# Kernel optimization log

Measured on AMD Instinct MI355X. Metric: run time of the kernel, lower is better.

Reference implementation:

```python
import jax, jax.numpy as jnp
import numpy as np

E, QE, P, H = 3, 60000, 40, 20   # elements, atoms per element, fp length, hidden
NIMG = 1800                       # images in batch
Q = E * QE                        # total atoms
NNZ = 14_400_000                  # nnz of sparse fprimes [P*Q, 3*Q]


def setup_inputs() -> dict:
    key = jax.random.key(0)
    ks = jax.random.split(key, 12)
    fps = jax.random.normal(ks[0], (E, QE, P), jnp.float32)
    image_idx = jax.random.randint(ks[1], (E, QE), 0, NIMG, jnp.int32)
    s1 = 1.0 / np.sqrt(P)
    s2 = 1.0 / np.sqrt(H)
    W1 = (jax.random.normal(ks[2], (E, P, H)) * s1).astype(jnp.float32)
    b1 = jnp.zeros((E, H), jnp.float32)
    W2 = (jax.random.normal(ks[3], (E, H, H)) * s2).astype(jnp.float32)
    b2 = jnp.zeros((E, H), jnp.float32)
    W3 = (jax.random.normal(ks[4], (E, H, 1)) * s2).astype(jnp.float32)
    b3 = jnp.zeros((E, 1), jnp.float32)
    fp_rows = jax.random.randint(ks[5], (NNZ,), 0, P * Q, jnp.int32)
    fp_cols = jax.random.randint(ks[6], (NNZ,), 0, 3 * Q, jnp.int32)
    fp_vals = (jax.random.normal(ks[7], (NNZ,)) * 0.05).astype(jnp.float32)
    return {"fps": fps, "W1": W1, "b1": b1, "W2": W2, "b2": b2, "W3": W3,
            "b3": b3, "image_idx": image_idx, "fp_rows": fp_rows,
            "fp_cols": fp_cols, "fp_vals": fp_vals, "batch_size": NIMG}


def _mlp(x, w1, b1, w2, b2, w3, b3):
    # Dense(tanh) -> Dense(tanh) -> Dense(linear), per amptorch MLP(n_layers=3)
    h = jnp.tanh(x @ w1 + b1)
    h = jnp.tanh(h @ w2 + b2)
    return h @ w3 + b3  # [..., 1]


def _esum(x, w1, b1, w2, b2, w3, b3):
    return _mlp(x, w1, b1, w2, b2, w3, b3).sum()


def reference(fps, W1, b1, W2, b2, W3, b3, image_idx, fp_rows, fp_cols,
              fp_vals, batch_size):
    # per-element atomwise energies: [E, QE, 1]
    atom_e = jax.vmap(_mlp)(fps, W1, b1, W2, b2, W3, b3)
    # scatter-add atomic energies into per-image energies (index_add_)
    energy_pred = jax.ops.segment_sum(
        atom_e.reshape(-1, 1), image_idx.reshape(-1).astype(jnp.int32),
        num_segments=batch_size)  # [NIMG, 1]
    # dE/dFP per atom (each atom's output depends only on its own fp, so
    # grad of the per-element energy sum == per-atom jacobian rows)
    dE_dFP = jax.vmap(jax.grad(_esum))(fps, W1, b1, W2, b2, W3, b3)  # [E,QE,P]
    # reorder atoms from element-grouped order to image-index order
    # (stable argsort == boolean-match reorder in the torch code)
    order = jnp.argsort(image_idx.reshape(-1))
    dE_flat = dE_dFP.reshape(-1, P)[order].reshape(-1)  # [P*Q]
    # force = -fprimes^T @ dE_dFP  (sparse COO matvec via segment_sum)
    force_flat = -jax.ops.segment_sum(
        fp_vals * dE_flat[fp_rows], fp_cols, num_segments=3 * Q)
    force_pred = force_flat.reshape(-1, 3)  # [Q, 3]
    return energy_pred, force_pred
```

## Files before the change

kernel.cpp:

```cpp
#include <hip/hip_runtime.h>
#include <math.h>

#define E_    3
#define QE_   60000
#define QTOT  180000
#define P_    40
#define H_    20
#define NIMG_ 1800
#define NNZ_  14400000
#define BLK   256
#define NB    704

#define CW_BITS 12
#define CW      4096
#define NBIN    132
#define SUBS    8
#define SC      8192
#define NSB     1758

typedef int   vi4 __attribute__((ext_vector_type(4)));
typedef float vf4 __attribute__((ext_vector_type(4)));

__global__ void zero_kernel(float* __restrict__ out, int n) {
    int i = blockIdx.x * blockDim.x + threadIdx.x;
    if (i < n) out[i] = 0.0f;
}

__global__ void hist_kernel(const int* __restrict__ img, int* __restrict__ g_hist) {
    __shared__ int h[NIMG_];
    const int t = threadIdx.x, b = blockIdx.x;
    for (int v = t; v < NIMG_; v += BLK) h[v] = 0;
    __syncthreads();
    int a = b * BLK + t;
    if (a < QTOT) atomicAdd(&h[img[a]], 1);
    __syncthreads();
    for (int v = t; v < NIMG_; v += BLK) g_hist[v * NB + b] = h[v];
}

__global__ void scan_blocks_kernel(int* __restrict__ g_hist, int* __restrict__ g_total) {
    __shared__ int s[BLK];
    const int v = blockIdx.x, t = threadIdx.x;
    int carry = 0;
    for (int c = 0; c < NB; c += BLK) {
        int idx = c + t;
        int val = (idx < NB) ? g_hist[v * NB + idx] : 0;
        s[t] = val; __syncthreads();
        for (int off = 1; off < BLK; off <<= 1) {
            int tmp = (t >= off) ? s[t - off] : 0;
            __syncthreads();
            s[t] += tmp;
            __syncthreads();
        }
        int excl = s[t] - val;
        int tot  = s[BLK - 1];
        if (idx < NB) g_hist[v * NB + idx] = carry + excl;
        carry += tot;
        __syncthreads();
    }
// ... 83 lines not shown
    float ea = sB3;
    #pragma unroll
    for (int i = 0; i < H_; ++i) ea += h2v[i] * sW3[i];
    atomicAdd(&energy[img[a]], ea);

    float dz2[H_];
    #pragma unroll
    for (int i = 0; i < H_; ++i) dz2[i] = sW3[i] * (1.0f - h2v[i] * h2v[i]);
    float dz1[H_];
    #pragma unroll
    for (int i = 0; i < H_; ++i) {
        float d = 0.0f;
        #pragma unroll
        for (int j = 0; j < H_; ++j) d += sW2[i * H_ + j] * dz2[j];
        dz1[i] = d * (1.0f - h1v[i] * h1v[i]);
    }
    float* op = dEflat + (size_t)rank[a] * P_;
    #pragma unroll
    for (int p = 0; p < P_; p += 4) {
        float4 v4;
        float d0 = 0.f, d1 = 0.f, d2 = 0.f, d3 = 0.f;
        #pragma unroll
        for (int i = 0; i < H_; ++i) {
            d0 += sW1[(p    ) * H_ + i] * dz1[i];
            d1 += sW1[(p + 1) * H_ + i] * dz1[i];
            d2 += sW1[(p + 2) * H_ + i] * dz1[i];
            d3 += sW1[(p + 3) * H_ + i] * dz1[i];
        }
        v4.x = d0; v4.y = d1; v4.z = d2; v4.w = d3;
        *(float4*)(op + p) = v4;
    }
}

__global__ __launch_bounds__(BLK) void fhist_kernel(const int* __restrict__ cols,
                                                    int* __restrict__ binHist) {
    __shared__ int h[NBIN];
    const int t = threadIdx.x, b = blockIdx.x;
    if (t < NBIN) h[t] = 0;
    __syncthreads();
    const int base = b * SC;
    if (base + SC <= NNZ_) {
        const vi4* c4 = (const vi4*)(cols + base);
        #pragma unroll
        for (int j = 0; j < SC / (BLK * 4); ++j) {
            vi4 cc = __builtin_nontemporal_load(c4 + j * BLK + t);
            atomicAdd(&h[cc.x >> CW_BITS], 1);
            atomicAdd(&h[cc.y >> CW_BITS], 1);
            atomicAdd(&h[cc.z >> CW_BITS], 1);
            atomicAdd(&h[cc.w >> CW_BITS], 1);
        }
    } else {
        for (int j = 0; j < SC / BLK; ++j) {
            int k = base + j * BLK + t;
            if (k < NNZ_) atomicAdd(&h[cols[k] >> CW_BITS], 1);
        }
    }
    __syncthreads();
    if (t < NBIN) binHist[t * NSB + b] = h[t];
}

__global__ void fscan_blocks_kernel(int* __restrict__ binHist, int* __restrict__ binTotal) {
    __shared__ int s[BLK];
    const int v = blockIdx.x, t = threadIdx.x;
    int carry = 0;
    for (int c = 0; c < NSB; c += BLK) {
        int idx = c + t;
        int val = (idx < NSB) ? binHist[v * NSB + idx] : 0;
        s[t] = val; __syncthreads();
        for (int off = 1; off < BLK; off <<= 1) {
            int tmp = (t >= off) ? s[t - off] : 0;
            __syncthreads();
            s[t] += tmp;
            __syncthreads();
        }
        int excl = s[t] - val;
        int tot  = s[BLK - 1];
        if (idx < NSB) binHist[v * NSB + idx] = carry + excl;
        carry += tot;
        __syncthreads();
    }
    if (t == 0) binTotal[v] = carry;
}

__global__ void fbase_kernel(const int* __restrict__ binTotal, int* __restrict__ binBase) {
    __shared__ int s[BLK];
    const int t = threadIdx.x;
    int v = (t < NBIN) ? binTotal[t] : 0;
    s[t] = v; __syncthreads();
    for (int off = 1; off < BLK; off <<= 1) {
        int tmp = (t >= off) ? s[t - off] : 0;
        __syncthreads();
        s[t] += tmp;
        __syncthreads();
    }
    if (t < NBIN) binBase[t] = s[t] - v;
    if (t == 0) binBase[NBIN] = s[BLK - 1];
}

__global__ __launch_bounds__(BLK) void fscatter_kernel(
    const int* __restrict__ rows, const int* __restrict__ cols, const float* __restrict__ vals,
    const float* __restrict__ dEflat, const int* __restrict__ binHist,
    const int* __restrict__ binBase, unsigned* __restrict__ bm)
{
    __shared__ unsigned items[SC];
    __shared__ unsigned char bins[SC];
    __shared__ int hist[NBIN];
    __shared__ int cursor[NBIN];
    __shared__ int delta[NBIN];
    __shared__ int s[BLK];
    const int t = threadIdx.x, b = blockIdx.x;
    const int base = b * SC;
    const int nIt = min(SC, NNZ_ - base);
    const bool full = (base + SC <= NNZ_);

    if (t < NBIN) hist[t] = 0;
    __syncthreads();

    if (full) {
        const vi4* c4 = (const vi4*)(cols + base);
        #pragma unroll
        for (int j = 0; j < SC / (BLK * 4); ++j) {
            vi4 cc = __builtin_nontemporal_load(c4 + j * BLK + t);
            atomicAdd(&hist[cc.x >> CW_BITS], 1);
            atomicAdd(&hist[cc.y >> CW_BITS], 1);
            atomicAdd(&hist[cc.z >> CW_BITS], 1);
            atomicAdd(&hist[cc.w >> CW_BITS], 1);
        }
    } else {
        for (int j = 0; j < SC / BLK; ++j) {
            int k = base + j * BLK + t;
            if (k < NNZ_) atomicAdd(&hist[cols[k] >> CW_BITS], 1);
        }
    }
    __syncthreads();

    {
        int v = (t < NBIN) ? hist[t] : 0;
        s[t] = v; __syncthreads();
        for (int off = 1; off < BLK; off <<= 1) {
            int tmp = (t >= off) ? s[t - off] : 0;
            __syncthreads();
            s[t] += tmp;
            __syncthreads();
        }
        if (t < NBIN) {
            int ls = s[t] - v;
            cursor[t] = ls;
            delta[t]  = binBase[t] + binHist[t * NSB + b] - ls;
        }
    }
    __syncthreads();

    if (full) {
        const vi4* c4 = (const vi4*)(cols + base);
        const vi4* r4 = (const vi4*)(rows + base);
        const vf4* v4 = (const vf4*)(vals + base);
        #pragma unroll 2
        for (int j = 0; j < SC / (BLK * 4); ++j) {
            int idx = j * BLK + t;
            vi4 cc = __builtin_nontemporal_load(c4 + idx);
            vi4 rr = __builtin_nontemporal_load(r4 + idx);
            vf4 vv = __builtin_nontemporal_load(v4 + idx);
            float d0 = dEflat[rr.x];
            float d1 = dEflat[rr.y];
            float d2 = dEflat[rr.z];
            float d3 = dEflat[rr.w];
            #define PLACE(CI, VI, DI)                                              \
            {                                                                      \
                int bin = (CI) >> CW_BITS;                                         \
                unsigned u = __float_as_uint(-(VI) * (DI));                        \
                unsigned pk = ((unsigned)((CI) & (CW - 1)) << 20)                  \
                            | ((u + 0x800u) >> 12);                                \
                int pos = atomicAdd(&cursor[bin], 1);                              \
                items[pos] = pk;                                                   \
                bins[pos] = (unsigned char)bin;                                    \
            }
            PLACE(cc.x, vv.x, d0)
            PLACE(cc.y, vv.y, d1)
            PLACE(cc.z, vv.z, d2)
            PLACE(cc.w, vv.w, d3)
        }
    } else {
        for (int j = 0; j < SC / BLK; ++j) {
            int k = base + j * BLK + t;
            if (k < NNZ_) {
                int c = cols[k];
                float d = dEflat[rows[k]];
                float v = vals[k];
                PLACE(c, v, d)
            }
        }
    }
    __syncthreads();

    for (int i = t; i < nIt; i += BLK) {
        __builtin_nontemporal_store(items[i], &bm[delta[bins[i]] + i]);
    }
}

__global__ __launch_bounds__(BLK) void fforce_kernel(
    const unsigned* __restrict__ bm, const int* __restrict__ binBase,
    float* __restrict__ partial)
{
    __shared__ float w[CW];
    const int t = threadIdx.x;
    const int bin = blockIdx.x >> 3;
    const int sub = blockIdx.x & (SUBS - 1);
    for (int i = t; i < CW; i += BLK) w[i] = 0.0f;
    __syncthreads();
    const int start = binBase[bin];
    const int cnt   = binBase[bin + 1] - start;
    const int sBeg  = start + (cnt * sub) / SUBS;
    const int sEnd  = start + (cnt * (sub + 1)) / SUBS;
    int i = sBeg + t;
    for (; i + 3 * BLK < sEnd; i += 4 * BLK) {
        unsigned p0 = __builtin_nontemporal_load(bm + i);
        unsigned p1 = __builtin_nontemporal_load(bm + i + BLK);
        unsigned p2 = __builtin_nontemporal_load(bm + i + 2 * BLK);
        unsigned p3 = __builtin_nontemporal_load(bm + i + 3 * BLK);
        atomicAdd(&w[p0 >> 20], __uint_as_float((p0 & 0xFFFFFu) << 12));
        atomicAdd(&w[p1 >> 20], __uint_as_float((p1 & 0xFFFFFu) << 12));
        atomicAdd(&w[p2 >> 20], __uint_as_float((p2 & 0xFFFFFu) << 12));
        atomicAdd(&w[p3 >> 20], __uint_as_float((p3 & 0xFFFFFu) << 12));
    }
    for (; i < sEnd; i += BLK) {
        unsigned p = bm[i];
        atomicAdd(&w[p >> 20], __uint_as_float((p & 0xFFFFFu) << 12));
    }
    __syncthreads();
    float* dst = partial + (size_t)blockIdx.x * CW;
    for (int k = t; k < CW; k += BLK) __builtin_nontemporal_store(w[k], dst + k);
}

__global__ void freduce_kernel(const float* __restrict__ partial, float* __restrict__ force) {
    int i = blockIdx.x * BLK + threadIdx.x;
    if (i < 3 * QTOT) {
        int bin = i >> CW_BITS, local = i & (CW - 1);
        const float* p = partial + (size_t)bin * (CW * SUBS) + local;
        float sum = 0.0f;
        #pragma unroll
        for (int k = 0; k < SUBS; ++k) sum += __builtin_nontemporal_load(p + k * CW);
        force[i] = sum;
    }
}

__global__ void force_kernel(const int* __restrict__ rows, const int* __restrict__ cols,
                             const float* __restrict__ vals, const float* __restrict__ dEflat,
                             float* __restrict__ force) {
    int k = blockIdx.x * blockDim.x + threadIdx.x;
    if (k < NNZ_) {
        float contrib = -vals[k] * dEflat[rows[k]];
        atomicAdd(&force[cols[k]], contrib);
    }
}

extern "C" void kernel_launch(void* const* d_in, const int* in_sizes, int n_in,
                              void* d_out, int out_size, void* d_ws, size_t ws_size,
                              hipStream_t stream) {
    (void)in_sizes; (void)n_in; (void)out_size;
    const float* fps  = (const float*)d_in[0];
    const float* W1   = (const float*)d_in[1];
    const float* b1   = (const float*)d_in[2];
    const float* W2   = (const float*)d_in[3];
    const float* b2   = (const float*)d_in[4];
    const float* W3   = (const float*)d_in[5];
    const float* b3   = (const float*)d_in[6];
    const int*   img  = (const int*)d_in[7];
    const int*   rows = (const int*)d_in[8];
    const int*   cols = (const int*)d_in[9];
    const float* vals = (const float*)d_in[10];

    char* ws = (char*)d_ws;
    int*   g_hist  = (int*)(ws);
    int*   g_total = (int*)(ws + 5068800);
    int*   g_base  = (int*)(ws + 5076000);
    int*   rank    = (int*)(ws + 5083200);
    float* dEflat  = (float*)(ws + 5803200);
    int*      binHist  = (int*)(ws + 34603200);
    int*      binTotal = (int*)(ws + 35531424);
    int*      binBase  = (int*)(ws + 35531952);
    unsigned* bm       = (unsigned*)(ws + 35532496);
    float*    partial  = (float*)(ws + 93132496);
    const size_t WS_NEEDED = 110434000;

    float* energy = (float*)d_out;
    float* force  = (float*)d_out + NIMG_;

    const int nOut = NIMG_ + 3 * QTOT;
    zero_kernel<<<(nOut + BLK - 1) / BLK, BLK, 0, stream>>>((float*)d_out, nOut);

    hist_kernel<<<NB, BLK, 0, stream>>>(img, g_hist);
    scan_blocks_kernel<<<NIMG_, BLK, 0, stream>>>(g_hist, g_total);
    scan_buckets_kernel<<<1, BLK, 0, stream>>>(g_total, g_base);
    rank_kernel<<<NB, BLK, 0, stream>>>(img, g_hist, g_base, rank);

    dim3 gm((QE_ + BLK - 1) / BLK, E_);
    mlp_kernel<<<gm, BLK, 0, stream>>>(fps, W1, b1, W2, b2, W3, b3, img, rank,
                                       energy, dEflat);

    if (ws_size >= WS_NEEDED) {
        fhist_kernel<<<NSB, BLK, 0, stream>>>(cols, binHist);
        fscan_blocks_kernel<<<NBIN, BLK, 0, stream>>>(binHist, binTotal);
        fbase_kernel<<<1, BLK, 0, stream>>>(binTotal, binBase);
        fscatter_kernel<<<NSB, BLK, 0, stream>>>(rows, cols, vals, dEflat,
                                                 binHist, binBase, bm);
        fforce_kernel<<<NBIN * SUBS, BLK, 0, stream>>>(bm, binBase, partial);
        freduce_kernel<<<(3 * QTOT + BLK - 1) / BLK, BLK, 0, stream>>>(partial, force);
    } else {
        force_kernel<<<NNZ_ / BLK, BLK, 0, stream>>>(rows, cols, vals, dEflat, force);
    }
}
```

Before: 647.7 us.

## Pre-sort nnz by row slice so dEflat gathers stay L2-local

Adds a new force path that first buckets nonzeros into 55 row slices (slice histogram, plan, per-block slice sort). Each entry is stored as a packed (15-bit value, local row) word plus its column. The column-binned scatter then runs per slice, with each group of blocks working on one slice, so the random dEflat gathers hit a small window that fits in cache. The cost is an extra full pass that reads and writes all 14.4M nnz, several more kernel launches, a larger workspace, and value precision cut to about 15 bits.

```diff
diff --git a/kernel.cpp b/kernel.cpp
--- a/kernel.cpp
+++ b/kernel.cpp
@@ -18,12 +18,33 @@
 #define SC      8192
 #define NSB     1758
 
+#define SLICE_SHIFT 17
+#define NSLICE  55
+#define MAXCH   1813
+#define FS_GRID 768
+#define FS_PERX 96
+
+#define C_CNT   0
+#define C_SBASE 64
+#define C_SCUR  128
+#define C_TOT   184
+#define C_CHS   192
+#define C_CHST  2048
+#define C_CHLEN 4096
+#define C_GRP   6144
+#define C_GCNT  8192
+#define C_INTS  8448
+
 typedef int   vi4 __attribute__((ext_vector_type(4)));
 typedef float vf4 __attribute__((ext_vector_type(4)));
+typedef unsigned uint32;
 
 __global__ void zero_kernel(float* __restrict__ out, int n) {
     int i = blockIdx.x * blockDim.x + threadIdx.x;
     if (i < n) out[i] = 0.0f;
+}
+__global__ void zero_ctrl_kernel(int* __restrict__ ctrl) {
+    ctrl[threadIdx.x] = 0;
 }
 
 __global__ void hist_kernel(const int* __restrict__ img, int* __restrict__ g_hist) {
@@ -173,40 +194,208 @@
     }
 }
 
-__global__ __launch_bounds__(BLK) void fhist_kernel(const int* __restrict__ cols,
-                                                    int* __restrict__ binHist) {
-    __shared__ int h[NBIN];
+
+__global__ __launch_bounds__(BLK) void slice_hist_kernel(const int* __restrict__ rows,
+                                                         int* __restrict__ ctrl) {
+    __shared__ int h[NSLICE];
     const int t = threadIdx.x, b = blockIdx.x;
-    if (t < NBIN) h[t] = 0;
+    if (t < NSLICE) h[t] = 0;
     __syncthreads();
     const int base = b * SC;
     if (base + SC <= NNZ_) {
-        const vi4* c4 = (const vi4*)(cols + base);
+        const vi4* r4 = (const vi4*)(rows + base);
         #pragma unroll
         for (int j = 0; j < SC / (BLK * 4); ++j) {
-            vi4 cc = __builtin_nontemporal_load(c4 + j * BLK + t);
-            atomicAdd(&h[cc.x >> CW_BITS], 1);
-            atomicAdd(&h[cc.y >> CW_BITS], 1);
-            atomicAdd(&h[cc.z >> CW_BITS], 1);
-            atomicAdd(&h[cc.w >> CW_BITS], 1);
+            vi4 rr = __builtin_nontemporal_load(r4 + j * BLK + t);
+            atomicAdd(&h[rr.x >> SLICE_SHIFT], 1);
+            atomicAdd(&h[rr.y >> SLICE_SHIFT], 1);
+            atomicAdd(&h[rr.z >> SLICE_SHIFT], 1);
+            atomicAdd(&h[rr.w >> SLICE_SHIFT], 1);
         }
     } else {
         for (int j = 0; j < SC / BLK; ++j) {
             int k = base + j * BLK + t;
-            if (k < NNZ_) atomicAdd(&h[cols[k] >> CW_BITS], 1);
-        }
-    }
-    __syncthreads();
-    if (t < NBIN) binHist[t * NSB + b] = h[t];
-}
-
-__global__ void fscan_blocks_kernel(int* __restrict__ binHist, int* __restrict__ binTotal) {
+            if (k < NNZ_) atomicAdd(&h[rows[k] >> SLICE_SHIFT], 1);
+        }
+    }
+    __syncthreads();
+    if (t < NSLICE && h[t] > 0) atomicAdd(&ctrl[C_CNT + t], h[t]);
+}
+
+__global__ void plan_kernel(int* __restrict__ ctrl) {
+    __shared__ int scnt[NSLICE], sb[NSLICE + 1], cb[NSLICE + 1], gp[NSLICE];
+    __shared__ int g8[8], tot_s;
+    const int t = threadIdx.x;
+    if (t < NSLICE) scnt[t] = ctrl[C_CNT + t];
+    __syncthreads();
+    if (t == 0) {
+        int run = 0, crun = 0;
+        int gs[8]; for (int x = 0; x < 8; ++x) gs[x] = 0;
+        for (int s = 0; s < NSLICE; ++s) {
+            sb[s] = run;
+            run += scnt[s];
+            run = (run + 3) & ~3;
+            int nc = (scnt[s] + SC - 1) / SC;
+            cb[s] = crun; crun += nc;
+            int x = s & 7;
+            gp[s] = gs[x]; gs[x] += nc;
+        }
+        sb[NSLICE] = run; cb[NSLICE] = crun; tot_s = crun;
+        for (int x = 0; x < 8; ++x) g8[x] = gs[x];
+    }
+    __syncthreads();
+    const int tot = tot_s;
+    if (t < NSLICE) { ctrl[C_SBASE + t] = sb[t]; ctrl[C_SCUR + t] = sb[t]; }
+    if (t == 0) { ctrl[C_SBASE + NSLICE] = sb[NSLICE]; ctrl[C_TOT] = tot; }
+    if (t < 8) ctrl[C_GCNT + t] = g8[t];
+    for (int idx = t; idx < MAXCH; idx += BLK) {
+        if (idx < tot) {
+            int s = 0;
+            for (int k = 0; k < NSLICE; ++k) if (cb[k] <= idx) s = k;
+            int c = idx - cb[s];
+            ctrl[C_CHS + idx]   = s;
+            ctrl[C_CHST + idx]  = sb[s] + c * SC;
+            ctrl[C_CHLEN + idx] = min(SC, scnt[s] - c * SC);
+            ctrl[C_GRP + (s & 7) * 256 + gp[s] + c] = idx;
+        } else {
+            ctrl[C_CHS + idx] = 0; ctrl[C_CHST + idx] = 0; ctrl[C_CHLEN + idx] = 0;
+        }
+    }
+}
+
+__global__ __launch_bounds__(BLK) void slice_sort_kernel(
+    const int* __restrict__ rows, const int* __restrict__ cols, const float* __restrict__ vals,
+    int* __restrict__ ctrl, uint32* __restrict__ itemX, uint32* __restrict__ itemY)
+{
+    __shared__ uint32 rbuf[SC];
+    __shared__ uint32 sbuf[SC];
+    __shared__ int h[NSLICE], lb[NSLICE + 1], res[NSLICE], cur[NSLICE];
+    const int t = threadIdx.x, b = blockIdx.x;
+    const int base = b * SC;
+    const int len = min(SC, NNZ_ - base);
+    const bool full = (len == SC);
+
+    if (t < NSLICE) h[t] = 0;
+    __syncthreads();
+    if (full) {
+        const vi4* r4 = (const vi4*)(rows + base);
+        #pragma unroll
+        for (int j = 0; j < SC / (BLK * 4); ++j) {
+            int idx = j * BLK + t;
+            vi4 rr = __builtin_nontemporal_load(r4 + idx);
+            rbuf[idx * 4 + 0] = (uint32)rr.x; atomicAdd(&h[rr.x >> SLICE_SHIFT], 1);
+            rbuf[idx * 4 + 1] = (uint32)rr.y; atomicAdd(&h[rr.y >> SLICE_SHIFT], 1);
+            rbuf[idx * 4 + 2] = (uint32)rr.z; atomicAdd(&h[rr.z >> SLICE_SHIFT], 1);
+            rbuf[idx * 4 + 3] = (uint32)rr.w; atomicAdd(&h[rr.w >> SLICE_SHIFT], 1);
+        }
+    } else {
+        for (int j = t; j < len; j += BLK) {
+            int r = rows[base + j];
+            rbuf[j] = (uint32)r;
+            atomicAdd(&h[r >> SLICE_SHIFT], 1);
+        }
+    }
+    __syncthreads();
+    if (t == 0) {
+        int run = 0;
+        for (int s = 0; s < NSLICE; ++s) { lb[s] = run; run += h[s]; }
+        lb[NSLICE] = run;
+    }
+    __syncthreads();
+    if (t < NSLICE) {
+        cur[t] = lb[t];
+        res[t] = (h[t] > 0) ? atomicAdd(&ctrl[C_SCUR + t], h[t]) : 0;
+    }
+    __syncthreads();
+    for (int j = t; j < len; j += BLK) {
+        uint32 r = rbuf[j];
+        int bn = (int)(r >> SLICE_SHIFT);
+        int pos = atomicAdd(&cur[bn], 1);
+        sbuf[pos] = ((uint32)j << SLICE_SHIFT) | (r & 0x1FFFFu);
+    }
+    __syncthreads();
+    if (full) {
+        const vi4* v4 = (const vi4*)(vals + base);
+        #pragma unroll
+        for (int j = 0; j < SC / (BLK * 4); ++j) {
+            int idx = j * BLK + t;
+            vi4 vv = __builtin_nontemporal_load(v4 + idx);
+            rbuf[idx * 4 + 0] = (uint32)vv.x; rbuf[idx * 4 + 1] = (uint32)vv.y;
+            rbuf[idx * 4 + 2] = (uint32)vv.z; rbuf[idx * 4 + 3] = (uint32)vv.w;
+        }
+    } else {
+        for (int j = t; j < len; j += BLK) rbuf[j] = ((const uint32*)vals)[base + j];
+    }
+    __syncthreads();
+    for (int j = t; j < len; j += BLK) {
+        uint32 e = sbuf[j];
+        int i = (int)(e >> SLICE_SHIFT);
+        uint32 rl = e & 0x1FFFFu;
+        uint32 v15 = (rbuf[i] + 0x10000u) >> 17;
+        int lo = 0, hi = NSLICE;
+        while (hi - lo > 1) { int mid = (lo + hi) >> 1; if (lb[mid] <= j) lo = mid; else hi = mid; }
+        int dst = res[lo] + (j - lb[lo]);
+        itemX[dst] = (v15 << 17) | rl;
+    }
+    __syncthreads();
+    if (full) {
+        const vi4* c4 = (const vi4*)(cols + base);
+        #pragma unroll
+        for (int j = 0; j < SC / (BLK * 4); ++j) {
+            int idx = j * BLK + t;
+            vi4 cc = __builtin_nontemporal_load(c4 + idx);
+            rbuf[idx * 4 + 0] = (uint32)cc.x; rbuf[idx * 4 + 1] = (uint32)cc.y;
+            rbuf[idx * 4 + 2] = (uint32)cc.z; rbuf[idx * 4 + 3] = (uint32)cc.w;
+        }
+    } else {
+        for (int j = t; j < len; j += BLK) rbuf[j] = (uint32)cols[base + j];
+    }
+    __syncthreads();
+    for (int j = t; j < len; j += BLK) {
+        uint32 e = sbuf[j];
+        int i = (int)(e >> SLICE_SHIFT);
+        int lo = 0, hi = NSLICE;
+        while (hi - lo > 1) { int mid = (lo + hi) >> 1; if (lb[mid] <= j) lo = mid; else hi = mid; }
+        int dst = res[lo] + (j - lb[lo]);
+        itemY[dst] = rbuf[i];
+    }
+}
+
+__global__ __launch_bounds__(BLK) void fhist3_kernel(const uint32* __restrict__ itemY,
+                                                     const int* __restrict__ ctrl,
+                                                     int* __restrict__ binHist) {
+    __shared__ int h[NBIN];
+    const int t = threadIdx.x, g = blockIdx.x;
+    if (t < NBIN) h[t] = 0;
+    __syncthreads();
+    const int start = ctrl[C_CHST + g];
+    const int len   = ctrl[C_CHLEN + g];
+    if (len == SC) {
+        const vi4* y4 = (const vi4*)(itemY + start);
+        #pragma unroll
+        for (int j = 0; j < SC / (BLK * 4); ++j) {
+            vi4 yy = __builtin_nontemporal_load(y4 + j * BLK + t);
+            atomicAdd(&h[yy.x >> CW_BITS], 1);
+            atomicAdd(&h[yy.y >> CW_BITS], 1);
+            atomicAdd(&h[yy.z >> CW_BITS], 1);
+            atomicAdd(&h[yy.w >> CW_BITS], 1);
+        }
+    } else {
+        for (int j = t; j < len; j += BLK)
+            atomicAdd(&h[itemY[start + j] >> CW_BITS], 1);
+    }
+    __syncthreads();
+    if (t < NBIN) binHist[t * MAXCH + g] = h[t];
+}
+
+__global__ void fscan_blocks_kernel(int* __restrict__ binHist, int* __restrict__ binTotal,
+                                    int n) {
     __shared__ int s[BLK];
     const int v = blockIdx.x, t = threadIdx.x;
     int carry = 0;
-    for (int c = 0; c < NSB; c += BLK) {
+    for (int c = 0; c < n; c += BLK) {
         int idx = c + t;
-        int val = (idx < NSB) ? binHist[v * NSB + idx] : 0;
+        int val = (idx < n) ? binHist[v * n + idx] : 0;
         s[t] = val; __syncthreads();
         for (int off = 1; off < BLK; off <<= 1) {
             int tmp = (t >= off) ? s[t - off] : 0;
@@ -216,7 +405,7 @@
         }
         int excl = s[t] - val;
         int tot  = s[BLK - 1];
-        if (idx < NSB) binHist[v * NSB + idx] = carry + excl;
+        if (idx < n) binHist[v * n + idx] = carry + excl;
         carry += tot;
         __syncthreads();
     }
@@ -238,12 +427,184 @@
     if (t == 0) binBase[NBIN] = s[BLK - 1];
 }
 
+__global__ __launch_bounds__(BLK) void fscatter3_kernel(
+    const uint32* __restrict__ itemX, const uint32* __restrict__ itemY,
+    const float* __restrict__ dEflat, const int* __restrict__ ctrl,
+    const int* __restrict__ binHist, const int* __restrict__ binBase,
+    uint32* __restrict__ bm)
+{
+    __shared__ uint32 items[SC];
+    __shared__ unsigned char bns[SC];
+    __shared__ int h[NBIN], cur[NBIN], dlt[NBIN];
+    __shared__ int sc[BLK];
+    const int t = threadIdx.x;
+    const int x = blockIdx.x & 7;
+    const int r = blockIdx.x >> 3;
+    const int gc = ctrl[C_GCNT + x];
+
+    for (int w = r; w < gc; w += FS_PERX) {
+        const int g     = ctrl[C_GRP + x * 256 + w];
+        const int sl    = ctrl[C_CHS + g];
+        const int start = ctrl[C_CHST + g];
+        const int len   = ctrl[C_CHLEN + g];
+        const int row0  = sl << SLICE_SHIFT;
+
+        if (t < NBIN) h[t] = 0;
+        __syncthreads();
+        if (len == SC) {
+            const vi4* y4 = (const vi4*)(itemY + start);
+            #pragma unroll
+            for (int j = 0; j < SC / (BLK * 4); ++j) {
+                vi4 yy = __builtin_nontemporal_load(y4 + j * BLK + t);
+                atomicAdd(&h[yy.x >> CW_BITS], 1);
+                atomicAdd(&h[yy.y >> CW_BITS], 1);
+                atomicAdd(&h[yy.z >> CW_BITS], 1);
+                atomicAdd(&h[yy.w >> CW_BITS], 1);
+            }
+        } else {
+            for (int j = t; j < len; j += BLK)
+                atomicAdd(&h[itemY[start + j] >> CW_BITS], 1);
+        }
+        __syncthreads();
+        {
+            int v = (t < NBIN) ? h[t] : 0;
+            sc[t] = v; __syncthreads();
+            for (int off = 1; off < BLK; off <<= 1) {
+                int tmp = (t >= off) ? sc[t - off] : 0;
+                __syncthreads();
+                sc[t] += tmp;
+                __syncthreads();
+            }
+            if (t < NBIN) {
+                int ls = sc[t] - v;
+                cur[t] = ls;
+                dlt[t] = binBase[t] + binHist[t * MAXCH + g] - ls;
+            }
+        }
+        __syncthreads();
+        if (len == SC) {
+            const vi4* x4 = (const vi4*)(itemX + start);
+            const vi4* y4 = (const vi4*)(itemY + start);
+            #pragma unroll 2
+            for (int j = 0; j < SC / (BLK * 4); ++j) {
+                int idx = j * BLK + t;
+                vi4 xx = __builtin_nontemporal_load(x4 + idx);
+                vi4 yy = __builtin_nontemporal_load(y4 + idx);
+                float d0 = dEflat[row0 + (((uint32)xx.x) & 0x1FFFFu)];
+                float d1 = dEflat[row0 + (((uint32)xx.y) & 0x1FFFFu)];
+                float d2 = dEflat[row0 + (((uint32)xx.z) & 0x1FFFFu)];
+                float d3 = dEflat[row0 + (((uint32)xx.w) & 0x1FFFFu)];
+                #define PLACE3(XI, YI, DI)                                         \
+                {                                                                  \
+                    uint32 col = (uint32)(YI);                                     \
+                    int bin = (int)(col >> CW_BITS);                               \
+                    float val = __uint_as_float((((uint32)(XI)) >> 17) << 17);     \
+                    uint32 u = __float_as_uint(-val * (DI));                       \
+                    uint32 pk = ((col & (CW - 1)) << 20) | ((u + 0x800u) >> 12);   \
+                    int pos = atomicAdd(&cur[bin], 1);                             \
+                    items[pos] = pk;                                               \
+                    bns[pos] = (unsigned char)bin;                                 \
+                }
+                PLACE3(xx.x, yy.x, d0)
+                PLACE3(xx.y, yy.y, d1)
+                PLACE3(xx.z, yy.z, d2)
+                PLACE3(xx.w, yy.w, d3)
+            }
+        } else {
+            for (int j = t; j < len; j += BLK) {
+                uint32 xi = itemX[start + j];
+                uint32 yi = itemY[start + j];
+                float d = dEflat[row0 + (xi & 0x1FFFFu)];
+                PLACE3(xi, yi, d)
+            }
+        }
+        __syncthreads();
+        for (int i = t; i < len; i += BLK) {
+            __builtin_nontemporal_store(items[i], &bm[dlt[bns[i]] + i]);
+        }
+        __syncthreads();
+    }
+}
+
+__global__ __launch_bounds__(BLK) void fforce_kernel(
+    const uint32* __restrict__ bm, const int* __restrict__ binBase,
+    float* __restrict__ partial)
+{
+    __shared__ float w[CW];
+    const int t = threadIdx.x;
+    const int bin = blockIdx.x >> 3;
+    const int sub = blockIdx.x & (SUBS - 1);
+    for (int i = t; i < CW; i += BLK) w[i] = 0.0f;
+    __syncthreads();
+    const int start = binBase[bin];
+    const int cnt   = binBase[bin + 1] - start;
+    const int sBeg  = start + (cnt * sub) / SUBS;
+    const int sEnd  = start + (cnt * (sub + 1)) / SUBS;
+    int i = sBeg + t;
+    for (; i + 3 * BLK < sEnd; i += 4 * BLK) {
+        uint32 p0 = __builtin_nontemporal_load(bm + i);
+        uint32 p1 = __builtin_nontemporal_load(bm + i + BLK);
+        uint32 p2 = __builtin_nontemporal_load(bm + i + 2 * BLK);
+        uint32 p3 = __builtin_nontemporal_load(bm + i + 3 * BLK);
+        atomicAdd(&w[p0 >> 20], __uint_as_float((p0 & 0xFFFFFu) << 12));
+        atomicAdd(&w[p1 >> 20], __uint_as_float((p1 & 0xFFFFFu) << 12));
+        atomicAdd(&w[p2 >> 20], __uint_as_float((p2 & 0xFFFFFu) << 12));
+        atomicAdd(&w[p3 >> 20], __uint_as_float((p3 & 0xFFFFFu) << 12));
+    }
+    for (; i < sEnd; i += BLK) {
+        uint32 p = bm[i];
+        atomicAdd(&w[p >> 20], __uint_as_float((p & 0xFFFFFu) << 12));
+    }
+    __syncthreads();
+    float* dst = partial + (size_t)blockIdx.x * CW;
+    for (int k = t; k < CW; k += BLK) __builtin_nontemporal_store(w[k], dst + k);
+}
+
+__global__ void freduce_kernel(const float* __restrict__ partial, float* __restrict__ force) {
+    int i = blockIdx.x * BLK + threadIdx.x;
+    if (i < 3 * QTOT) {
+        int bin = i >> CW_BITS, local = i & (CW - 1);
+        const float* p = partial + (size_t)bin * (CW * SUBS) + local;
+        float sum = 0.0f;
+        #pragma unroll
+        for (int k = 0; k < SUBS; ++k) sum += __builtin_nontemporal_load(p + k * CW);
+        force[i] = sum;
+    }
+}
+
+__global__ __launch_bounds__(BLK) void fhist_kernel(const int* __restrict__ cols,
+                                                    int* __restrict__ binHist) {
+    __shared__ int h[NBIN];
+    const int t = threadIdx.x, b = blockIdx.x;
+    if (t < NBIN) h[t] = 0;
+    __syncthreads();
+    const int base = b * SC;
+    if (base + SC <= NNZ_) {
+        const vi4* c4 = (const vi4*)(cols + base);
+        #pragma unroll
+        for (int j = 0; j < SC / (BLK * 4); ++j) {
+            vi4 cc = __builtin_nontemporal_load(c4 + j * BLK + t);
+            atomicAdd(&h[cc.x >> CW_BITS], 1);
+            atomicAdd(&h[cc.y >> CW_BITS], 1);
+            atomicAdd(&h[cc.z >> CW_BITS], 1);
+            atomicAdd(&h[cc.w >> CW_BITS], 1);
+        }
+    } else {
+        for (int j = 0; j < SC / BLK; ++j) {
+            int k = base + j * BLK + t;
+            if (k < NNZ_) atomicAdd(&h[cols[k] >> CW_BITS], 1);
+        }
+    }
+    __syncthreads();
+    if (t < NBIN) binHist[t * NSB + b] = h[t];
+}
+
 __global__ __launch_bounds__(BLK) void fscatter_kernel(
     const int* __restrict__ rows, const int* __restrict__ cols, const float* __restrict__ vals,
     const float* __restrict__ dEflat, const int* __restrict__ binHist,
-    const int* __restrict__ binBase, unsigned* __restrict__ bm)
+    const int* __restrict__ binBase, uint32* __restrict__ bm)
 {
-    __shared__ unsigned items[SC];
+    __shared__ uint32 items[SC];
     __shared__ unsigned char bins[SC];
     __shared__ int hist[NBIN];
     __shared__ int cursor[NBIN];
@@ -256,7 +617,6 @@
 
     if (t < NBIN) hist[t] = 0;
     __syncthreads();
-
     if (full) {
         const vi4* c4 = (const vi4*)(cols + base);
         #pragma unroll
@@ -274,7 +634,6 @@
         }
     }
     __syncthreads();
-
     {
         int v = (t < NBIN) ? hist[t] : 0;
         s[t] = v; __syncthreads();
@@ -291,7 +650,6 @@
         }
     }
     __syncthreads();
-
     if (full) {
         const vi4* c4 = (const vi4*)(cols + base);
         const vi4* r4 = (const vi4*)(rows + base);
@@ -309,8 +667,8 @@
             #define PLACE(CI, VI, DI)                                              \
             {                                                                      \
                 int bin = (CI) >> CW_BITS;                                         \
-                unsigned u = __float_as_uint(-(VI) * (DI));                        \
-                unsigned pk = ((unsigned)((CI) & (CW - 1)) << 20)                  \
+                uint32 u = __float_as_uint(-(VI) * (DI));                          \
+                uint32 pk = ((uint32)((CI) & (CW - 1)) << 20)                      \
                             | ((u + 0x800u) >> 12);                                \
                 int pos = atomicAdd(&cursor[bin], 1);                              \
                 items[pos] = pk;                                                   \
@@ -333,55 +691,8 @@
         }
     }
     __syncthreads();
-
     for (int i = t; i < nIt; i += BLK) {
         __builtin_nontemporal_store(items[i], &bm[delta[bins[i]] + i]);
-    }
-}
-
-__global__ __launch_bounds__(BLK) void fforce_kernel(
-    const unsigned* __restrict__ bm, const int* __restrict__ binBase,
-    float* __restrict__ partial)
-{
-    __shared__ float w[CW];
-    const int t = threadIdx.x;
-    const int bin = blockIdx.x >> 3;
-    const int sub = blockIdx.x & (SUBS - 1);
-    for (int i = t; i < CW; i += BLK) w[i] = 0.0f;
-    __syncthreads();
-    const int start = binBase[bin];
-    const int cnt   = binBase[bin + 1] - start;
-    const int sBeg  = start + (cnt * sub) / SUBS;
-    const int sEnd  = start + (cnt * (sub + 1)) / SUBS;
-    int i = sBeg + t;
-    for (; i + 3 * BLK < sEnd; i += 4 * BLK) {
-        unsigned p0 = __builtin_nontemporal_load(bm + i);
-        unsigned p1 = __builtin_nontemporal_load(bm + i + BLK);
-        unsigned p2 = __builtin_nontemporal_load(bm + i + 2 * BLK);
-        unsigned p3 = __builtin_nontemporal_load(bm + i + 3 * BLK);
-        atomicAdd(&w[p0 >> 20], __uint_as_float((p0 & 0xFFFFFu) << 12));
-        atomicAdd(&w[p1 >> 20], __uint_as_float((p1 & 0xFFFFFu) << 12));
-        atomicAdd(&w[p2 >> 20], __uint_as_float((p2 & 0xFFFFFu) << 12));
-        atomicAdd(&w[p3 >> 20], __uint_as_float((p3 & 0xFFFFFu) << 12));
-    }
-    for (; i < sEnd; i += BLK) {
-        unsigned p = bm[i];
-        atomicAdd(&w[p >> 20], __uint_as_float((p & 0xFFFFFu) << 12));
-    }
-    __syncthreads();
-    float* dst = partial + (size_t)blockIdx.x * CW;
-    for (int k = t; k < CW; k += BLK) __builtin_nontemporal_store(w[k], dst + k);
-}
-
-__global__ void freduce_kernel(const float* __restrict__ partial, float* __restrict__ force) {
-    int i = blockIdx.x * BLK + threadIdx.x;
-    if (i < 3 * QTOT) {
-        int bin = i >> CW_BITS, local = i & (CW - 1);
-        const float* p = partial + (size_t)bin * (CW * SUBS) + local;
-        float sum = 0.0f;
-        #pragma unroll
-        for (int k = 0; k < SUBS; ++k) sum += __builtin_nontemporal_load(p + k * CW);
-        force[i] = sum;
     }
 }
 
@@ -417,12 +728,6 @@
     int*   g_base  = (int*)(ws + 5076000);
     int*   rank    = (int*)(ws + 5083200);
     float* dEflat  = (float*)(ws + 5803200);
-    int*      binHist  = (int*)(ws + 34603200);
-    int*      binTotal = (int*)(ws + 35531424);
-    int*      binBase  = (int*)(ws + 35531952);
-    unsigned* bm       = (unsigned*)(ws + 35532496);
-    float*    partial  = (float*)(ws + 93132496);
-    const size_t WS_NEEDED = 110434000;
 
     float* energy = (float*)d_out;
     float* force  = (float*)d_out + NIMG_;
@@ -439,14 +744,43 @@
     mlp_kernel<<<gm, BLK, 0, stream>>>(fps, W1, b1, W2, b2, W3, b3, img, rank,
                                        energy, dEflat);
 
-    if (ws_size >= WS_NEEDED) {
-        fhist_kernel<<<NSB, BLK, 0, stream>>>(cols, binHist);
-        fscan_blocks_kernel<<<NBIN, BLK, 0, stream>>>(binHist, binTotal);
-        fbase_kernel<<<1, BLK, 0, stream>>>(binTotal, binBase);
+    int*    binHist3  = (int*)(ws + 34603200);
+    int*    binTotal3 = (int*)(ws + 35560464);
+    int*    binBase3  = (int*)(ws + 35560992);
+    int*    ctrl      = (int*)(ws + 35563136);
+    uint32* itemX     = (uint32*)(ws + 35596928);
+    uint32* itemY     = (uint32*)(ws + 93198976);
+    uint32* bm3       = (uint32*)(ws + 150801024);
+    float*  partial3  = (float*)(ws + 35596928);
+    const size_t WS_V3 = 208401024;
+
+    int*    binHist5  = (int*)(ws + 34603200);
+    int*    binTotal5 = (int*)(ws + 35531424);
+    int*    binBase5  = (int*)(ws + 35531952);
+    uint32* bm5       = (uint32*)(ws + 35532496);
+    float*  partial5  = (float*)(ws + 93132496);
+    const size_t WS_V2 = 110434000;
+
+    if (ws_size >= WS_V3) {
+        zero_ctrl_kernel<<<1, 256, 0, stream>>>(ctrl);
+        slice_hist_kernel<<<NSB, BLK, 0, stream>>>(rows, ctrl);
+        plan_kernel<<<1, BLK, 0, stream>>>(ctrl);
+        slice_sort_kernel<<<NSB, BLK, 0, stream>>>(rows, cols, vals, ctrl, itemX, itemY);
+        fhist3_kernel<<<MAXCH, BLK, 0, stream>>>(itemY, ctrl, binHist3);
+        fscan_blocks_kernel<<<NBIN, BLK, 0, stream>>>(binHist3, binTotal3, MAXCH);
+        fbase_kernel<<<1, BLK, 0, stream>>>(binTotal3, binBase3);
+        fscatter3_kernel<<<FS_GRID, BLK, 0, stream>>>(itemX, itemY, dEflat, ctrl,
+                                                      binHist3, binBase3, bm3);
+        fforce_kernel<<<NBIN * SUBS, BLK, 0, stream>>>(bm3, binBase3, partial3);
+        freduce_kernel<<<(3 * QTOT + BLK - 1) / BLK, BLK, 0, stream>>>(partial3, force);
+    } else if (ws_size >= WS_V2) {
+        fhist_kernel<<<NSB, BLK, 0, stream>>>(cols, binHist5);
+        fscan_blocks_kernel<<<NBIN, BLK, 0, stream>>>(binHist5, binTotal5, NSB);
+        fbase_kernel<<<1, BLK, 0, stream>>>(binTotal5, binBase5);
         fscatter_kernel<<<NSB, BLK, 0, stream>>>(rows, cols, vals, dEflat,
-                                                 binHist, binBase, bm);
-        fforce_kernel<<<NBIN * SUBS, BLK, 0, stream>>>(bm, binBase, partial);
-        freduce_kernel<<<(3 * QTOT + BLK - 1) / BLK, BLK, 0, stream>>>(partial, force);
+                                                 binHist5, binBase5, bm5);
+        fforce_kernel<<<NBIN * SUBS, BLK, 0, stream>>>(bm5, binBase5, partial5);
+        freduce_kernel<<<(3 * QTOT + BLK - 1) / BLK, BLK, 0, stream>>>(partial5, force);
     } else {
         force_kernel<<<NNZ_ / BLK, BLK, 0, stream>>>(rows, cols, vals, dEflat, force);
     }
```

New measurement: 711.9 us. 1.1x slower.

## Pre-partition sparse entries by row slice to localize dE gathers

Applied to the files above, without the earlier changes.

Adds a first pass that buckets the COO entries by row slice (128K rows each) into a packed uint2 buffer. The value is truncated to 15 bits and stored with the low row bits. A planning kernel then splits each slice into chunks, and the column-binning scatter reads these chunks so that dEflat lookups stay within a small, cache-resident window instead of gathering randomly across the whole array. Global atomic cursors replace the separate column-histogram and scan passes. The cost is an extra ~115MB write and reread of intermediate items, lower precision for the values, and a larger workspace requirement that falls back to the old path if it is not available.

```diff
diff --git a/kernel.cpp b/kernel.cpp
--- a/kernel.cpp
+++ b/kernel.cpp
@@ -18,12 +18,33 @@
 #define SC      8192
 #define NSB     1758
 
+#define SLICE_SHIFT 17
+#define NSLICE  55
+#define CAPS    270336
+#define CAPB    114688
+#define MAXCH4  1815
+#define FS_GRID 768
+#define FS_PERX 96
+
+#define C_SCUR  0
+#define C_BCUR  64
+#define C_GCNT  256
+#define C_CHS   512
+#define C_CHST  2432
+#define C_CHLEN 4352
+#define C_GRP   6272
+#define C_INTS  8320
+
 typedef int   vi4 __attribute__((ext_vector_type(4)));
 typedef float vf4 __attribute__((ext_vector_type(4)));
+typedef unsigned uint32;
 
 __global__ void zero_kernel(float* __restrict__ out, int n) {
     int i = blockIdx.x * blockDim.x + threadIdx.x;
     if (i < n) out[i] = 0.0f;
+}
+__global__ void zero_ctrl_kernel(int* __restrict__ ctrl) {
+    ctrl[threadIdx.x] = 0;
 }
 
 __global__ void hist_kernel(const int* __restrict__ img, int* __restrict__ g_hist) {
@@ -173,6 +194,246 @@
     }
 }
 
+
+__global__ __launch_bounds__(BLK) void slice_scatter_kernel(
+    const int* __restrict__ rows, const int* __restrict__ cols, const float* __restrict__ vals,
+    int* __restrict__ ctrl, uint2* __restrict__ items)
+{
+    __shared__ uint32 srow[SC];
+    __shared__ int h[NSLICE], lcur[NSLICE], gbase[NSLICE];
+    const int t = threadIdx.x, b = blockIdx.x;
+    const int base = b * SC;
+    const int len = min(SC, NNZ_ - base);
+    const bool full = (len == SC);
+
+    if (t < NSLICE) h[t] = 0;
+    __syncthreads();
+    if (full) {
+        const vi4* r4 = (const vi4*)(rows + base);
+        #pragma unroll
+        for (int j = 0; j < SC / (BLK * 4); ++j) {
+            int idx = j * BLK + t;
+            vi4 rr = __builtin_nontemporal_load(r4 + idx);
+            srow[idx * 4 + 0] = (uint32)rr.x; atomicAdd(&h[rr.x >> SLICE_SHIFT], 1);
+            srow[idx * 4 + 1] = (uint32)rr.y; atomicAdd(&h[rr.y >> SLICE_SHIFT], 1);
+            srow[idx * 4 + 2] = (uint32)rr.z; atomicAdd(&h[rr.z >> SLICE_SHIFT], 1);
+            srow[idx * 4 + 3] = (uint32)rr.w; atomicAdd(&h[rr.w >> SLICE_SHIFT], 1);
+        }
+    } else {
+        for (int j = t; j < len; j += BLK) {
+            int r = rows[base + j];
+            srow[j] = (uint32)r;
+            atomicAdd(&h[r >> SLICE_SHIFT], 1);
+        }
+    }
+    __syncthreads();
+    if (t < NSLICE) {
+        lcur[t] = 0;
+        gbase[t] = (h[t] > 0) ? atomicAdd(&ctrl[C_SCUR + t], h[t]) : 0;
+    }
+    __syncthreads();
+    if (full) {
+        const vi4* c4 = (const vi4*)(cols + base);
+        const vi4* v4 = (const vf4*)(vals + base) ? (const vi4*)(vals + base) : nullptr;
+        #pragma unroll 2
+        for (int j = 0; j < SC / (BLK * 4); ++j) {
+            int idx = j * BLK + t;
+            vi4 cc = __builtin_nontemporal_load(c4 + idx);
+            vi4 vv = __builtin_nontemporal_load(v4 + idx);
+            #define EMIT(K, CI, VB)                                                \
+            {                                                                      \
+                uint32 r = srow[idx * 4 + K];                                      \
+                int sl = (int)(r >> SLICE_SHIFT);                                  \
+                int pos = gbase[sl] + atomicAdd(&lcur[sl], 1);                     \
+                uint32 v15 = (((uint32)(VB)) + 0x10000u) >> 17;                    \
+                items[(size_t)sl * CAPS + pos] =                                   \
+                    make_uint2((v15 << 17) | (r & 0x1FFFFu), (uint32)(CI));        \
+            }
+            EMIT(0, cc.x, vv.x)
+            EMIT(1, cc.y, vv.y)
+            EMIT(2, cc.z, vv.z)
+            EMIT(3, cc.w, vv.w)
+        }
+    } else {
+        for (int j = t; j < len; j += BLK) {
+            uint32 r = srow[j];
+            int sl = (int)(r >> SLICE_SHIFT);
+            int pos = gbase[sl] + atomicAdd(&lcur[sl], 1);
+            uint32 vb = ((const uint32*)vals)[base + j];
+            uint32 v15 = (vb + 0x10000u) >> 17;
+            items[(size_t)sl * CAPS + pos] =
+                make_uint2((v15 << 17) | (r & 0x1FFFFu), (uint32)cols[base + j]);
+        }
+    }
+}
+
+__global__ void plan4_kernel(int* __restrict__ ctrl) {
+    __shared__ int scnt[NSLICE], cb[NSLICE + 1], gp[NSLICE];
+    __shared__ int g8[8], tot_s;
+    const int t = threadIdx.x;
+    if (t < NSLICE) scnt[t] = ctrl[C_SCUR + t];
+    __syncthreads();
+    if (t == 0) {
+        int crun = 0;
+        int gs[8]; for (int x = 0; x < 8; ++x) gs[x] = 0;
+        for (int s = 0; s < NSLICE; ++s) {
+            int nc = (scnt[s] + SC - 1) / SC;
+            cb[s] = crun; crun += nc;
+            int x = s & 7;
+            gp[s] = gs[x]; gs[x] += nc;
+        }
+        cb[NSLICE] = crun; tot_s = crun;
+        for (int x = 0; x < 8; ++x) g8[x] = gs[x];
+    }
+    __syncthreads();
+    const int tot = tot_s;
+    if (t < 8) ctrl[C_GCNT + t] = g8[t];
+    for (int idx = t; idx < tot; idx += BLK) {
+        int s = 0;
+        for (int k = 0; k < NSLICE; ++k) if (cb[k] <= idx) s = k;
+        int c = idx - cb[s];
+        ctrl[C_CHS + idx]   = s;
+        ctrl[C_CHST + idx]  = s * CAPS + c * SC;
+        ctrl[C_CHLEN + idx] = min(SC, scnt[s] - c * SC);
+        ctrl[C_GRP + (s & 7) * 256 + gp[s] + c] = idx;
+    }
+}
+
+__global__ __launch_bounds__(BLK) void fscatter4_kernel(
+    const uint2* __restrict__ items, const float* __restrict__ dEflat,
+    int* __restrict__ ctrl, uint32* __restrict__ bm)
+{
+    __shared__ uint32 itl[SC];
+    __shared__ unsigned char bns[SC];
+    __shared__ int h[NBIN], cur[NBIN], dlt[NBIN];
+    __shared__ int sc[BLK];
+    const int t = threadIdx.x;
+    const int x = blockIdx.x & 7;
+    const int r = blockIdx.x >> 3;
+    const int gc = ctrl[C_GCNT + x];
+
+    for (int w = r; w < gc; w += FS_PERX) {
+        const int g     = ctrl[C_GRP + x * 256 + w];
+        const int sl    = ctrl[C_CHS + g];
+        const int start = ctrl[C_CHST + g];
+        const int len   = ctrl[C_CHLEN + g];
+        const int row0  = sl << SLICE_SHIFT;
+        const int lenE  = len & ~1;
+
+        if (t < NBIN) h[t] = 0;
+        __syncthreads();
+        if (len == SC) {
+            const vi4* p4 = (const vi4*)(items + start);
+            #pragma unroll
+            for (int j = 0; j < SC / (BLK * 2); ++j) {
+                vi4 q = __builtin_nontemporal_load(p4 + j * BLK + t);
+                atomicAdd(&h[((uint32)q.y) >> CW_BITS], 1);
+                atomicAdd(&h[((uint32)q.w) >> CW_BITS], 1);
+            }
+        } else {
+            for (int j = t; j < len; j += BLK)
+                atomicAdd(&h[items[start + j].y >> CW_BITS], 1);
+        }
+        __syncthreads();
+        {
+            int v = (t < NBIN) ? h[t] : 0;
+            sc[t] = v; __syncthreads();
+            for (int off = 1; off < BLK; off <<= 1) {
+                int tmp = (t >= off) ? sc[t - off] : 0;
+                __syncthreads();
+                sc[t] += tmp;
+                __syncthreads();
+            }
+            if (t < NBIN) {
+                int ls = sc[t] - v;
+                cur[t] = ls;
+                int gb = (v > 0) ? atomicAdd(&ctrl[C_BCUR + t], v) : 0;
+                dlt[t] = t * CAPB + gb - ls;
+            }
+        }
+        __syncthreads();
+        #define PLACE4(LO, CO, DI)                                             \
+        {                                                                      \
+            uint32 col = (uint32)(CO);                                         \
+            int bin = (int)(col >> CW_BITS);                                   \
+            float val = __uint_as_float((((uint32)(LO)) >> 17) << 17);         \
+            uint32 u = __float_as_uint(-val * (DI));                           \
+            uint32 pk = ((col & (CW - 1)) << 20) | ((u + 0x800u) >> 12);       \
+            int pos = atomicAdd(&cur[bin], 1);                                 \
+            itl[pos] = pk;                                                     \
+            bns[pos] = (unsigned char)bin;                                     \
+        }
+        if (len == SC) {
+            const vi4* p4 = (const vi4*)(items + start);
+            #pragma unroll 2
+            for (int j = 0; j < SC / (BLK * 2); ++j) {
+                vi4 q = __builtin_nontemporal_load(p4 + j * BLK + t);
+                float dA = dEflat[row0 + (((uint32)q.x) & 0x1FFFFu)];
+                float dB = dEflat[row0 + (((uint32)q.z) & 0x1FFFFu)];
+                PLACE4(q.x, q.y, dA)
+                PLACE4(q.z, q.w, dB)
+            }
+        } else {
+            for (int j = t; j < len; j += BLK) {
+                uint2 it = items[start + j];
+                float d = dEflat[row0 + (it.x & 0x1FFFFu)];
+                PLACE4(it.x, it.y, d)
+            }
+        }
+        __syncthreads();
+        for (int i = t; i < len; i += BLK) {
+            __builtin_nontemporal_store(itl[i], &bm[dlt[bns[i]] + i]);
+        }
+        __syncthreads();
+    }
+}
+
+__global__ __launch_bounds__(BLK) void fforce4_kernel(
+    const uint32* __restrict__ bm, const int* __restrict__ ctrl,
+    float* __restrict__ partial)
+{
+    __shared__ float w[CW];
+    const int t = threadIdx.x;
+    const int bin = blockIdx.x >> 3;
+    const int sub = blockIdx.x & (SUBS - 1);
+    for (int i = t; i < CW; i += BLK) w[i] = 0.0f;
+    __syncthreads();
+    const int cnt   = ctrl[C_BCUR + bin];
+    const int start = bin * CAPB;
+    const int sBeg  = start + (cnt * sub) / SUBS;
+    const int sEnd  = start + (cnt * (sub + 1)) / SUBS;
+    int i = sBeg + t;
+    for (; i + 3 * BLK < sEnd; i += 4 * BLK) {
+        uint32 p0 = __builtin_nontemporal_load(bm + i);
+        uint32 p1 = __builtin_nontemporal_load(bm + i + BLK);
+        uint32 p2 = __builtin_nontemporal_load(bm + i + 2 * BLK);
+        uint32 p3 = __builtin_nontemporal_load(bm + i + 3 * BLK);
+        atomicAdd(&w[p0 >> 20], __uint_as_float((p0 & 0xFFFFFu) << 12));
+        atomicAdd(&w[p1 >> 20], __uint_as_float((p1 & 0xFFFFFu) << 12));
+        atomicAdd(&w[p2 >> 20], __uint_as_float((p2 & 0xFFFFFu) << 12));
+        atomicAdd(&w[p3 >> 20], __uint_as_float((p3 & 0xFFFFFu) << 12));
+    }
+    for (; i < sEnd; i += BLK) {
+        uint32 p = bm[i];
+        atomicAdd(&w[p >> 20], __uint_as_float((p & 0xFFFFFu) << 12));
+    }
+    __syncthreads();
+    float* dst = partial + (size_t)blockIdx.x * CW;
+    for (int k = t; k < CW; k += BLK) __builtin_nontemporal_store(w[k], dst + k);
+}
+
+__global__ void freduce_kernel(const float* __restrict__ partial, float* __restrict__ force) {
+    int i = blockIdx.x * BLK + threadIdx.x;
+    if (i < 3 * QTOT) {
+        int bin = i >> CW_BITS, local = i & (CW - 1);
+        const float* p = partial + (size_t)bin * (CW * SUBS) + local;
+        float sum = 0.0f;
+        #pragma unroll
+        for (int k = 0; k < SUBS; ++k) sum += __builtin_nontemporal_load(p + k * CW);
+        force[i] = sum;
+    }
+}
+
 __global__ __launch_bounds__(BLK) void fhist_kernel(const int* __restrict__ cols,
                                                     int* __restrict__ binHist) {
     __shared__ int h[NBIN];
@@ -200,13 +461,14 @@
     if (t < NBIN) binHist[t * NSB + b] = h[t];
 }
 
-__global__ void fscan_blocks_kernel(int* __restrict__ binHist, int* __restrict__ binTotal) {
+__global__ void fscan_blocks_kernel(int* __restrict__ binHist, int* __restrict__ binTotal,
+                                    int n) {
     __shared__ int s[BLK];
     const int v = blockIdx.x, t = threadIdx.x;
     int carry = 0;
-    for (int c = 0; c < NSB; c += BLK) {
+    for (int c = 0; c < n; c += BLK) {
         int idx = c + t;
-        int val = (idx < NSB) ? binHist[v * NSB + idx] : 0;
+        int val = (idx < n) ? binHist[v * n + idx] : 0;
         s[t] = val; __syncthreads();
         for (int off = 1; off < BLK; off <<= 1) {
             int tmp = (t >= off) ? s[t - off] : 0;
@@ -216,7 +478,7 @@
         }
         int excl = s[t] - val;
         int tot  = s[BLK - 1];
-        if (idx < NSB) binHist[v * NSB + idx] = carry + excl;
+        if (idx < n) binHist[v * n + idx] = carry + excl;
         carry += tot;
         __syncthreads();
     }
@@ -241,9 +503,9 @@
 __global__ __launch_bounds__(BLK) void fscatter_kernel(
     const int* __restrict__ rows, const int* __restrict__ cols, const float* __restrict__ vals,
     const float* __restrict__ dEflat, const int* __restrict__ binHist,
-    const int* __restrict__ binBase, unsigned* __restrict__ bm)
+    const int* __restrict__ binBase, uint32* __restrict__ bm)
 {
-    __shared__ unsigned items[SC];
+    __shared__ uint32 items[SC];
     __shared__ unsigned char bins[SC];
     __shared__ int hist[NBIN];
     __shared__ int cursor[NBIN];
@@ -256,7 +518,6 @@
 
     if (t < NBIN) hist[t] = 0;
     __syncthreads();
-
     if (full) {
         const vi4* c4 = (const vi4*)(cols + base);
         #pragma unroll
@@ -274,7 +535,6 @@
         }
     }
     __syncthreads();
-
     {
         int v = (t < NBIN) ? hist[t] : 0;
         s[t] = v; __syncthreads();
@@ -291,7 +551,6 @@
         }
     }
     __syncthreads();
-
     if (full) {
         const vi4* c4 = (const vi4*)(cols + base);
         const vi4* r4 = (const vi4*)(rows + base);
@@ -309,8 +568,8 @@
             #define PLACE(CI, VI, DI)                                              \
             {                                                                      \
                 int bin = (CI) >> CW_BITS;                                         \
-                unsigned u = __float_as_uint(-(VI) * (DI));                        \
-                unsigned pk = ((unsigned)((CI) & (CW - 1)) << 20)                  \
+                uint32 u = __float_as_uint(-(VI) * (DI));                          \
+                uint32 pk = ((uint32)((CI) & (CW - 1)) << 20)                      \
                             | ((u + 0x800u) >> 12);                                \
                 int pos = atomicAdd(&cursor[bin], 1);                              \
                 items[pos] = pk;                                                   \
@@ -333,14 +592,13 @@
         }
     }
     __syncthreads();
-
     for (int i = t; i < nIt; i += BLK) {
         __builtin_nontemporal_store(items[i], &bm[delta[bins[i]] + i]);
     }
 }
 
 __global__ __launch_bounds__(BLK) void fforce_kernel(
-    const unsigned* __restrict__ bm, const int* __restrict__ binBase,
+    const uint32* __restrict__ bm, const int* __restrict__ binBase,
     float* __restrict__ partial)
 {
     __shared__ float w[CW];
@@ -355,34 +613,22 @@
     const int sEnd  = start + (cnt * (sub + 1)) / SUBS;
     int i = sBeg + t;
     for (; i + 3 * BLK < sEnd; i += 4 * BLK) {
-        unsigned p0 = __builtin_nontemporal_load(bm + i);
-        unsigned p1 = __builtin_nontemporal_load(bm + i + BLK);
-        unsigned p2 = __builtin_nontemporal_load(bm + i + 2 * BLK);
-        unsigned p3 = __builtin_nontemporal_load(bm + i + 3 * BLK);
+        uint32 p0 = __builtin_nontemporal_load(bm + i);
+        uint32 p1 = __builtin_nontemporal_load(bm + i + BLK);
+        uint32 p2 = __builtin_nontemporal_load(bm + i + 2 * BLK);
+        uint32 p3 = __builtin_nontemporal_load(bm + i + 3 * BLK);
         atomicAdd(&w[p0 >> 20], __uint_as_float((p0 & 0xFFFFFu) << 12));
         atomicAdd(&w[p1 >> 20], __uint_as_float((p1 & 0xFFFFFu) << 12));
         atomicAdd(&w[p2 >> 20], __uint_as_float((p2 & 0xFFFFFu) << 12));
         atomicAdd(&w[p3 >> 20], __uint_as_float((p3 & 0xFFFFFu) << 12));
     }
     for (; i < sEnd; i += BLK) {
-        unsigned p = bm[i];
+        uint32 p = bm[i];
         atomicAdd(&w[p >> 20], __uint_as_float((p & 0xFFFFFu) << 12));
     }
     __syncthreads();
     float* dst = partial + (size_t)blockIdx.x * CW;
     for (int k = t; k < CW; k += BLK) __builtin_nontemporal_store(w[k], dst + k);
-}
-
-__global__ void freduce_kernel(const float* __restrict__ partial, float* __restrict__ force) {
-    int i = blockIdx.x * BLK + threadIdx.x;
-    if (i < 3 * QTOT) {
-        int bin = i >> CW_BITS, local = i & (CW - 1);
-        const float* p = partial + (size_t)bin * (CW * SUBS) + local;
-        float sum = 0.0f;
-        #pragma unroll
-        for (int k = 0; k < SUBS; ++k) sum += __builtin_nontemporal_load(p + k * CW);
-        force[i] = sum;
-    }
 }
 
 __global__ void force_kernel(const int* __restrict__ rows, const int* __restrict__ cols,
@@ -412,22 +658,32 @@
     const float* vals = (const float*)d_in[10];
 
     char* ws = (char*)d_ws;
-    int*   g_hist  = (int*)(ws);
-    int*   g_total = (int*)(ws + 5068800);
-    int*   g_base  = (int*)(ws + 5076000);
-    int*   rank    = (int*)(ws + 5083200);
-    float* dEflat  = (float*)(ws + 5803200);
-    int*      binHist  = (int*)(ws + 34603200);
-    int*      binTotal = (int*)(ws + 35531424);
-    int*      binBase  = (int*)(ws + 35531952);
-    unsigned* bm       = (unsigned*)(ws + 35532496);
-    float*    partial  = (float*)(ws + 93132496);
-    const size_t WS_NEEDED = 110434000;
-
     float* energy = (float*)d_out;
     float* force  = (float*)d_out + NIMG_;
-
     const int nOut = NIMG_ + 3 * QTOT;
+
+    int*    g_hist  = (int*)(ws);
+    int*    g_total = (int*)(ws + 5068800);
+    int*    g_base  = (int*)(ws + 5076000);
+    int*    rank    = (int*)(ws + 5083200);
+    uint2*  items   = (uint2*)(ws);
+    float*  partial4= (float*)(ws);
+    uint32* bm4     = (uint32*)(ws + 118947840);
+    int*    ctrl    = (int*)(ws + 179503104);
+    float*  dEflat4 = (float*)(ws + 179536384);
+    const size_t WS_V4 = 208336384;
+
+    float*  dEflat5   = (float*)(ws + 5803200);
+    int*    binHist5  = (int*)(ws + 34603200);
+    int*    binTotal5 = (int*)(ws + 35531424);
+    int*    binBase5  = (int*)(ws + 35531952);
+    uint32* bm5       = (uint32*)(ws + 35532496);
+    float*  partial5  = (float*)(ws + 93132496);
+    const size_t WS_V2 = 110434000;
+
+    const bool v4 = (ws_size >= WS_V4);
+    float* dEflat = v4 ? dEflat4 : dEflat5;
+
     zero_kernel<<<(nOut + BLK - 1) / BLK, BLK, 0, stream>>>((float*)d_out, nOut);
 
     hist_kernel<<<NB, BLK, 0, stream>>>(img, g_hist);
@@ -439,14 +695,21 @@
     mlp_kernel<<<gm, BLK, 0, stream>>>(fps, W1, b1, W2, b2, W3, b3, img, rank,
                                        energy, dEflat);
 
-    if (ws_size >= WS_NEEDED) {
-        fhist_kernel<<<NSB, BLK, 0, stream>>>(cols, binHist);
-        fscan_blocks_kernel<<<NBIN, BLK, 0, stream>>>(binHist, binTotal);
-        fbase_kernel<<<1, BLK, 0, stream>>>(binTotal, binBase);
+    if (v4) {
+        zero_ctrl_kernel<<<1, 256, 0, stream>>>(ctrl);
+        slice_scatter_kernel<<<NSB, BLK, 0, stream>>>(rows, cols, vals, ctrl, items);
+        plan4_kernel<<<1, BLK, 0, stream>>>(ctrl);
+        fscatter4_kernel<<<FS_GRID, BLK, 0, stream>>>(items, dEflat, ctrl, bm4);
+        fforce4_kernel<<<NBIN * SUBS, BLK, 0, stream>>>(bm4, ctrl, partial4);
+        freduce_kernel<<<(3 * QTOT + BLK - 1) / BLK, BLK, 0, stream>>>(partial4, force);
+    } else if (ws_size >= WS_V2) {
+        fhist_kernel<<<NSB, BLK, 0, stream>>>(cols, binHist5);
+        fscan_blocks_kernel<<<NBIN, BLK, 0, stream>>>(binHist5, binTotal5, NSB);
+        fbase_kernel<<<1, BLK, 0, stream>>>(binTotal5, binBase5);
         fscatter_kernel<<<NSB, BLK, 0, stream>>>(rows, cols, vals, dEflat,
-                                                 binHist, binBase, bm);
-        fforce_kernel<<<NBIN * SUBS, BLK, 0, stream>>>(bm, binBase, partial);
-        freduce_kernel<<<(3 * QTOT + BLK - 1) / BLK, BLK, 0, stream>>>(partial, force);
+                                                 binHist5, binBase5, bm5);
+        fforce_kernel<<<NBIN * SUBS, BLK, 0, stream>>>(bm5, binBase5, partial5);
+        freduce_kernel<<<(3 * QTOT + BLK - 1) / BLK, BLK, 0, stream>>>(partial5, force);
     } else {
         force_kernel<<<NNZ_ / BLK, BLK, 0, stream>>>(rows, cols, vals, dEflat, force);
     }
```

Measured after the change: 604.4 us. 1.07x faster.
